# Kernel tuning notes

Measured on AMD Instinct MI355X. Metric: run time of the kernel, lower is better.

The kernel has to match this reference:

```python
import jax, jax.numpy as jnp
import numpy as np

N_NODES = 50000
N_EDGES = 800000
D = 128
BN_EPS = 1e-5
AGG_EPS = 1e-6


def setup_inputs() -> dict:
    key = jax.random.key(0)
    ks = jax.random.split(key, 20)
    s = 1.0 / np.sqrt(D)
    def w(k):
        return jax.random.normal(k, (D, D), jnp.float32) * s
    def b(k):
        return jax.random.normal(k, (D,), jnp.float32) * 0.01
    return {
        "x": jax.random.normal(ks[0], (N_NODES, D), jnp.float32),
        "e": jax.random.normal(ks[1], (N_EDGES, D), jnp.float32),
        "edge_index": jax.random.randint(ks[2], (2, N_EDGES), 0, N_NODES, jnp.int32),
        "WA": w(ks[3]), "bA": b(ks[4]),
        "WB": w(ks[5]), "bB": b(ks[6]),
        "WC": w(ks[7]), "bC": b(ks[8]),
        "WD": w(ks[9]), "bD": b(ks[10]),
        "WE": w(ks[11]), "bE": b(ks[12]),
        "gamma_x": jnp.ones((D,), jnp.float32), "beta_x": jnp.zeros((D,), jnp.float32),
        "gamma_e": jnp.ones((D,), jnp.float32), "beta_e": jnp.zeros((D,), jnp.float32),
    }


def _batchnorm(v, gamma, beta):
    # training-mode BatchNorm1d: batch stats, biased variance
    mean = v.mean(axis=0)
    var = v.var(axis=0)
    return gamma * (v - mean) * jax.lax.rsqrt(var + BN_EPS) + beta


def reference(x, e, edge_index, WA, bA, WB, bB, WC, bC, WD, bD, WE, bE,
              gamma_x, beta_x, gamma_e, beta_e):
    n_nodes = x.shape[0]
    src = edge_index[0]  # x_j (source)
    dst = edge_index[1]  # x_i (target), aggregation index

    Ax = x @ WA + bA
    Bx = x @ WB + bB
    Ce = e @ WC + bC
    Dx = x @ WD + bD
    Ex = x @ WE + bE

    # message: gather endpoints, gate
    e_ij = Dx[dst] + Ex[src] + Ce            # [n_edges, D]
    sigma_ij = jax.nn.sigmoid(e_ij)

    # aggregate: scatter-sum numerator & denominator, normalize
    num = jax.ops.segment_sum(sigma_ij * Bx[src], dst, num_segments=n_nodes)
    den = jax.ops.segment_sum(sigma_ij, dst, num_segments=n_nodes)
    aggr = num / (den + AGG_EPS)

    # update + BN + ReLU (dropout=0, residual=False per GraphGym wrapper)
    x_out = jax.nn.relu(_batchnorm(Ax + aggr, gamma_x, beta_x))
    e_out = jax.nn.relu(_batchnorm(e_ij, gamma_e, beta_e))
    return x_out, e_out
```

## Files before the change

kernel.cpp:

```cpp
#include <hip/hip_runtime.h>
#include <stdint.h>

#define DD 128
#define NB_G 2048

using f32x4  = __attribute__((ext_vector_type(4))) float;
using bf16x8 = __attribute__((ext_vector_type(8))) short;

__device__ __forceinline__ float bf2f(short u) {
  union { unsigned int i; float f; } c;
  c.i = ((unsigned int)(unsigned short)u) << 16;
  return c.f;
}
__device__ __forceinline__ short f2bf(float f) {
  union { float f; unsigned int i; } c;
  c.f = f;
  unsigned int u = c.i;
  u += 0x7fffu + ((u >> 16) & 1u);
  return (short)(u >> 16);
}

__global__ __launch_bounds__(256) void k_hist(const int* __restrict__ dst, int* __restrict__ deg, int E) {
  int e = blockIdx.x * 256 + threadIdx.x;
  if (e < E) atomicAdd(&deg[dst[e]], 1);
}

__global__ __launch_bounds__(256) void k_scan1(const int* __restrict__ deg, int* __restrict__ off,
                                               int* __restrict__ totals, int n) {
  __shared__ int sm[256];
  int t = threadIdx.x;
  int i = blockIdx.x * 256 + t;
  int v = (i < n) ? deg[i] : 0;
  sm[t] = v;
  __syncthreads();
  int acc = v;
  #pragma unroll
  for (int d = 1; d < 256; d <<= 1) {
    int add = (t >= d) ? sm[t - d] : 0;
    __syncthreads();
    acc += add;
    sm[t] = acc;
    __syncthreads();
  }
  if (i < n) off[i] = acc - v;
  if (t == 255) totals[blockIdx.x] = acc;
}

__global__ __launch_bounds__(256) void k_scan2(const int* __restrict__ totals, int* __restrict__ boff, int nb) {
  __shared__ int sm[256];
  int t = threadIdx.x;
  int v = (t < nb) ? totals[t] : 0;
  sm[t] = v;
  __syncthreads();
  int acc = v;
  #pragma unroll
  for (int d = 1; d < 256; d <<= 1) {
    int add = (t >= d) ? sm[t - d] : 0;
    __syncthreads();
    acc += add;
    sm[t] = acc;
    __syncthreads();
  }
  boff[t] = acc - v;
}

__global__ __launch_bounds__(256) void k_scan3(int* __restrict__ off, const int* __restrict__ boff,
                                               int* __restrict__ cursor, int n) {
  int i = blockIdx.x * 256 + threadIdx.x;
  if (i < n) {
    int o = off[i] + boff[blockIdx.x];
    off[i] = o;
    cursor[i] = o;
  }
}

__global__ __launch_bounds__(256) void k_fill(const int* __restrict__ dst, const int* __restrict__ src,
                                              int* __restrict__ cursor, int* __restrict__ list,
                                              int* __restrict__ srcS, int* __restrict__ posOf, int E) {
  int e = blockIdx.x * 256 + threadIdx.x;
  if (e < E) {
    int p = atomicAdd(&cursor[dst[e]], 1);
    list[p] = e;
    srcS[p] = src[e];
    posOf[e] = p;
  }
}

__global__ __launch_bounds__(256) void k_nodegemm(
    const float* __restrict__ x,
    const float* __restrict__ WA, const float* __restrict__ bA,
    const float* __restrict__ WB, const float* __restrict__ bB,
    const float* __restrict__ WD, const float* __restrict__ bD,
    const float* __restrict__ WE, const float* __restrict__ bE,
    short* __restrict__ Axh, short* __restrict__ Bxh,
    short* __restrict__ Dxh, short* __restrict__ Exh, int n) {
  __shared__ __align__(16) short xs[64][136];
  __shared__ __align__(16) short wt[128][136];
  int t = threadIdx.x;
  int m0 = blockIdx.x * 64;

  for (int i = t; i < 64 * 32; i += 256) {
    int r = i >> 5, c4 = (i & 31) * 4;
    int gr = m0 + r;
    if (gr >= n) gr = n - 1;
    float4 v = *(const float4*)&x[(size_t)gr * DD + c4];
    xs[r][c4 + 0] = f2bf(v.x); xs[r][c4 + 1] = f2bf(v.y);
    xs[r][c4 + 2] = f2bf(v.z); xs[r][c4 + 3] = f2bf(v.w);
  }

  const float* Ws[4] = {WA, WB, WD, WE};
  const float* bs[4] = {bA, bB, bD, bE};
  short* Os[4] = {Axh, Bxh, Dxh, Exh};

  int l = t & 63, w = t >> 6, lg = l >> 4, lc = l & 15;

  #pragma unroll
  for (int wi = 0; wi < 4; ++wi) {
    __syncthreads();
    {
      int c = t & 127, kb = (t >> 7) * 8;
      const float* W = Ws[wi];
      for (int p = 0; p < 8; ++p) {
        int k0 = p * 16 + kb;
        bf16x8 v;
        #pragma unroll
        for (int j = 0; j < 8; ++j) v[j] = f2bf(W[(size_t)(k0 + j) * DD + c]);
        *(bf16x8*)&wt[c][k0] = v;
      }
    }
    __syncthreads();

    f32x4 acc[8] = {};
    #pragma unroll
    for (int kk = 0; kk < 4; ++kk) {
      bf16x8 af = *(const bf16x8*)&xs[w * 16 + lc][kk * 32 + lg * 8];
      #pragma unroll
      for (int tt = 0; tt < 8; ++tt) {
        bf16x8 bfv = *(const bf16x8*)&wt[tt * 16 + lc][kk * 32 + lg * 8];
        acc[tt] = __builtin_amdgcn_mfma_f32_16x16x32_bf16(af, bfv, acc[tt], 0, 0, 0);
      }
    }
    short* O = Os[wi];
    #pragma unroll
    for (int tt = 0; tt < 8; ++tt) {
      int col = tt * 16 + lc;
      float bv = bs[wi][col];
      #pragma unroll
      for (int j = 0; j < 4; ++j) {
        int row = m0 + w * 16 + lg * 4 + j;
        if (row < n) O[(size_t)row * DD + col] = f2bf(acc[tt][j] + bv);
      }
    }
  }
}

__global__ __launch_bounds__(256) void k_edge(
    const float* __restrict__ e, const float* __restrict__ WC, const float* __restrict__ bC,
    const int* __restrict__ srcI, const int* __restrict__ dstI, const int* __restrict__ posOf,
    const short* __restrict__ Dxh, const short* __restrict__ Exh,
    short* __restrict__ eijS, int Etot) {
  __shared__ __align__(16) short es[64][136];
  __shared__ __align__(16) short wt[128][136];
  int t = threadIdx.x;
  size_t m0 = (size_t)blockIdx.x * 64;

  for (int i = t; i < 64 * 32; i += 256) {
    int r = i >> 5, c4 = (i & 31) * 4;
    size_t gr = m0 + r;
    if (gr >= (size_t)Etot) gr = Etot - 1;
    float4 v = *(const float4*)&e[gr * DD + c4];
    es[r][c4 + 0] = f2bf(v.x); es[r][c4 + 1] = f2bf(v.y);
    es[r][c4 + 2] = f2bf(v.z); es[r][c4 + 3] = f2bf(v.w);
  }
  {
    int c = t & 127, kb = (t >> 7) * 8;
    for (int p = 0; p < 8; ++p) {
      int k0 = p * 16 + kb;
      bf16x8 v;
      #pragma unroll
      for (int j = 0; j < 8; ++j) v[j] = f2bf(WC[(size_t)(k0 + j) * DD + c]);
      *(bf16x8*)&wt[c][k0] = v;
    }
  }
  __syncthreads();

  int l = t & 63, w = t >> 6, lg = l >> 4, lc = l & 15;
  f32x4 acc[8] = {};
  #pragma unroll
  for (int kk = 0; kk < 4; ++kk) {
    bf16x8 af = *(const bf16x8*)&es[w * 16 + lc][kk * 32 + lg * 8];
    #pragma unroll
    for (int tt = 0; tt < 8; ++tt) {
      bf16x8 bfv = *(const bf16x8*)&wt[tt * 16 + lc][kk * 32 + lg * 8];
      acc[tt] = __builtin_amdgcn_mfma_f32_16x16x32_bf16(af, bfv, acc[tt], 0, 0, 0);
    }
  }
  float bCv[8];
  #pragma unroll
  for (int tt = 0; tt < 8; ++tt) bCv[tt] = bC[tt * 16 + lc];

  __syncthreads();
  #pragma unroll
  for (int tt = 0; tt < 8; ++tt) {
    int col = tt * 16 + lc;
    #pragma unroll
    for (int j = 0; j < 4; ++j)
      es[w * 16 + lg * 4 + j][col] = f2bf(acc[tt][j] + bCv[tt]);
  }
  __syncthreads();

  int rr = t >> 4, cl = (t & 15) * 8;
  #pragma unroll
  for (int p = 0; p < 4; ++p) {
    int r = rr + p * 16;
    size_t edge = m0 + r;
    if (edge < (size_t)Etot) {
      int dn = dstI[edge], sn = srcI[edge], pos = posOf[edge];
      bf16x8 cv = *(const bf16x8*)&es[r][cl];
      bf16x8 dv = *(const bf16x8*)&Dxh[(size_t)dn * DD + cl];
      bf16x8 sv = *(const bf16x8*)&Exh[(size_t)sn * DD + cl];
      bf16x8 o;
      #pragma unroll
      for (int j = 0; j < 8; ++j) o[j] = f2bf(bf2f(cv[j]) + bf2f(dv[j]) + bf2f(sv[j]));
      *(bf16x8*)&eijS[(size_t)pos * DD + cl] = o;
    }
  }
}

__global__ __launch_bounds__(256) void k_gather(
    const int* __restrict__ off, const int* __restrict__ deg, const int* __restrict__ srcS,
    const short* __restrict__ eijS, const short* __restrict__ Bxh, const short* __restrict__ Axh,
    float* __restrict__ outx, float* __restrict__ pE, float* __restrict__ pX, int n) {
  int t = threadIdx.x;
  int w = t >> 6, l = t & 63;
  int qw = l >> 4, fi = l & 15;
  int waveId = blockIdx.x * 4 + w;
  const int nwaves = NB_G * 4;

  float se[8] = {}, qe[8] = {};
  float sx[4] = {}, qx[4] = {};

  for (int node = waveId; node < n; node += nwaves) {
    int start = off[node], dg = deg[node];
    float num[8] = {}, den[8] = {};
    int k = qw;
    for (; k + 4 < dg; k += 8) {
      int p0 = start + k, p1 = start + k + 4;
      int s0 = srcS[p0], s1 = srcS[p1];
      bf16x8 e0 = *(const bf16x8*)&eijS[(size_t)p0 * DD + fi * 8];
      bf16x8 e1 = *(const bf16x8*)&eijS[(size_t)p1 * DD + fi * 8];
      bf16x8 b0 = *(const bf16x8*)&Bxh[(size_t)s0 * DD + fi * 8];
      bf16x8 b1 = *(const bf16x8*)&Bxh[(size_t)s1 * DD + fi * 8];
      #pragma unroll
      for (int j = 0; j < 8; ++j) {
        float v0 = bf2f(e0[j]), v1 = bf2f(e1[j]);
        float g0 = 1.f / (1.f + __expf(-v0)), g1 = 1.f / (1.f + __expf(-v1));
        num[j] += g0 * bf2f(b0[j]) + g1 * bf2f(b1[j]);
        den[j] += g0 + g1;
        se[j] += v0 + v1; qe[j] += v0 * v0 + v1 * v1;
      }
    }
    for (; k < dg; k += 4) {
      int p0 = start + k;
      int s0 = srcS[p0];
      bf16x8 e0 = *(const bf16x8*)&eijS[(size_t)p0 * DD + fi * 8];
      bf16x8 b0 = *(const bf16x8*)&Bxh[(size_t)s0 * DD + fi * 8];
      #pragma unroll
      for (int j = 0; j < 8; ++j) {
        float v0 = bf2f(e0[j]);
        float g0 = 1.f / (1.f + __expf(-v0));
        num[j] += g0 * bf2f(b0[j]);
        den[j] += g0;
        se[j] += v0; qe[j] += v0 * v0;
      }
    }
    #pragma unroll
    for (int j = 0; j < 8; ++j) {
      num[j] += __shfl_xor(num[j], 16); num[j] += __shfl_xor(num[j], 32);
      den[j] += __shfl_xor(den[j], 16); den[j] += __shfl_xor(den[j], 32);
    }
    if (qw < 2) {
      int c0 = fi * 8 + qw * 4;
      short4 ax = *(const short4*)&Axh[(size_t)node * DD + c0];
      short axa[4] = {ax.x, ax.y, ax.z, ax.w};
      float4 o;
      float vv[4];
      #pragma unroll
      for (int j = 0; j < 4; ++j) {
        int jj = qw * 4 + j;
        float aggr = num[jj] / (den[jj] + 1e-6f);
        float xp = bf2f(axa[j]) + aggr;
        vv[j] = xp;
        sx[j] += xp; qx[j] += xp * xp;
      }
      o.x = vv[0]; o.y = vv[1]; o.z = vv[2]; o.w = vv[3];
      *(float4*)&outx[(size_t)node * DD + c0] = o;
    }
  }

  #pragma unroll
  for (int j = 0; j < 8; ++j) {
    se[j] += __shfl_xor(se[j], 16); se[j] += __shfl_xor(se[j], 32);
    qe[j] += __shfl_xor(qe[j], 16); qe[j] += __shfl_xor(qe[j], 32);
  }
  __shared__ float lsE[4][128], lqE[4][128], lsX[4][128], lqX[4][128];
  if (qw == 0) {
    #pragma unroll
    for (int j = 0; j < 8; ++j) { lsE[w][fi * 8 + j] = se[j]; lqE[w][fi * 8 + j] = qe[j]; }
  }
  if (qw < 2) {
    #pragma unroll
    for (int j = 0; j < 4; ++j) { lsX[w][fi * 8 + qw * 4 + j] = sx[j]; lqX[w][fi * 8 + qw * 4 + j] = qx[j]; }
  }
  __syncthreads();
  if (t < 128) {
    float a = lsE[0][t] + lsE[1][t] + lsE[2][t] + lsE[3][t];
    float b = lqE[0][t] + lqE[1][t] + lqE[2][t] + lqE[3][t];
    pE[(size_t)blockIdx.x * 256 + t] = a;
    pE[(size_t)blockIdx.x * 256 + 128 + t] = b;
  } else {
    int c = t - 128;
    float a = lsX[0][c] + lsX[1][c] + lsX[2][c] + lsX[3][c];
    float b = lqX[0][c] + lqX[1][c] + lqX[2][c] + lqX[3][c];
    pX[(size_t)blockIdx.x * 256 + c] = a;
    pX[(size_t)blockIdx.x * 256 + 128 + c] = b;
  }
}

__global__ __launch_bounds__(256) void k_reduce(const float* __restrict__ part, int nblk, float invcnt,
                                                const float* __restrict__ gamma, const float* __restrict__ beta,
                                                float* __restrict__ stats) {
  int c = blockIdx.x, t = threadIdx.x;
  float a = 0.f, b = 0.f;
  for (int k = t; k < nblk; k += 256) {
    a += part[(size_t)k * 256 + c];
    b += part[(size_t)k * 256 + 128 + c];
  }
  #pragma unroll
  for (int o = 32; o > 0; o >>= 1) { a += __shfl_down(a, o); b += __shfl_down(b, o); }
  __shared__ float ra[4], rb[4];
  int l = t & 63, w = t >> 6;
  if (l == 0) { ra[w] = a; rb[w] = b; }
  __syncthreads();
  if (t == 0) {
    a = ra[0] + ra[1] + ra[2] + ra[3];
    b = rb[0] + rb[1] + rb[2] + rb[3];
    float mean = a * invcnt;
    float var = b * invcnt - mean * mean;
    float istd = rsqrtf(var + 1e-5f);
    float scale = gamma[c] * istd;
    stats[c] = scale;
    stats[128 + c] = beta[c] - mean * scale;
  }
}

__global__ __launch_bounds__(256) void k_xfinal(float* __restrict__ v, const float* __restrict__ st, size_t n4) {
  size_t i = (size_t)blockIdx.x * 256 + threadIdx.x;
  if (i >= n4) return;
  float4 d = *(const float4*)&v[i * 4];
  int f0 = (int)((i * 4) & 127);
  d.x = fmaxf(0.f, d.x * st[f0 + 0] + st[128 + f0 + 0]);
  d.y = fmaxf(0.f, d.y * st[f0 + 1] + st[128 + f0 + 1]);
  d.z = fmaxf(0.f, d.z * st[f0 + 2] + st[128 + f0 + 2]);
  d.w = fmaxf(0.f, d.w * st[f0 + 3] + st[128 + f0 + 3]);
  *(float4*)&v[i * 4] = d;
}

__global__ __launch_bounds__(256) void k_efinal(const short* __restrict__ eijS, const int* __restrict__ list,
                                                const float* __restrict__ st, float* __restrict__ out, int E) {
  int t = threadIdx.x;
  int pos = blockIdx.x * 16 + (t >> 4);
  if (pos >= E) return;
  int cl = (t & 15) * 8;
  int row = list[pos];
  bf16x8 u = *(const bf16x8*)&eijS[(size_t)pos * DD + cl];
  float4 s0 = *(const float4*)&st[cl], s1 = *(const float4*)&st[cl + 4];
  float4 h0 = *(const float4*)&st[128 + cl], h1 = *(const float4*)&st[128 + cl + 4];
  float4 a, b;
  a.x = fmaxf(0.f, bf2f(u[0]) * s0.x + h0.x);
  a.y = fmaxf(0.f, bf2f(u[1]) * s0.y + h0.y);
  a.z = fmaxf(0.f, bf2f(u[2]) * s0.z + h0.z);
  a.w = fmaxf(0.f, bf2f(u[3]) * s0.w + h0.w);
  b.x = fmaxf(0.f, bf2f(u[4]) * s1.x + h1.x);
  b.y = fmaxf(0.f, bf2f(u[5]) * s1.y + h1.y);
  b.z = fmaxf(0.f, bf2f(u[6]) * s1.z + h1.z);
  b.w = fmaxf(0.f, bf2f(u[7]) * s1.w + h1.w);
  *(float4*)&out[(size_t)row * DD + cl] = a;
  *(float4*)&out[(size_t)row * DD + cl + 4] = b;
}

extern "C" void kernel_launch(void* const* d_in, const int* in_sizes, int n_in,
                              void* d_out, int out_size, void* d_ws, size_t ws_size,
                              hipStream_t stream) {
  const float* x  = (const float*)d_in[0];
  const float* e  = (const float*)d_in[1];
  const int*   ei = (const int*)d_in[2];
  const float* WA = (const float*)d_in[3];  const float* bA = (const float*)d_in[4];
  const float* WB = (const float*)d_in[5];  const float* bB = (const float*)d_in[6];
  const float* WC = (const float*)d_in[7];  const float* bC = (const float*)d_in[8];
  const float* WD = (const float*)d_in[9];  const float* bD = (const float*)d_in[10];
  const float* WE = (const float*)d_in[11]; const float* bE = (const float*)d_in[12];
  const float* gx = (const float*)d_in[13]; const float* bx = (const float*)d_in[14];
  const float* ge = (const float*)d_in[15]; const float* be = (const float*)d_in[16];

  int N = in_sizes[0] / DD;
  int E = in_sizes[2] / 2;
  const int* srcI = ei;
  const int* dstI = ei + E;

  float* outx = (float*)d_out;
  float* oute = (float*)d_out + (size_t)N * DD;

  char* wp = (char*)d_ws;
  auto alloc = [&](size_t sz) { char* p = wp; wp += (sz + 255) & ~(size_t)255; return p; };
  short* Axh    = (short*)alloc((size_t)N * DD * 2);
  short* Bxh    = (short*)alloc((size_t)N * DD * 2);
  short* Dxh    = (short*)alloc((size_t)N * DD * 2);
  short* Exh    = (short*)alloc((size_t)N * DD * 2);
  short* eijS   = (short*)alloc((size_t)E * DD * 2);
  int*   deg    = (int*)alloc((size_t)N * 4);
  int*   off    = (int*)alloc((size_t)N * 4);
  int*   cursor = (int*)alloc((size_t)N * 4);
  int*   totals = (int*)alloc(1024);
  int*   boff   = (int*)alloc(1024);
  int*   list   = (int*)alloc((size_t)E * 4);
  int*   srcS   = (int*)alloc((size_t)E * 4);
  int*   posOf  = (int*)alloc((size_t)E * 4);
  float* pE     = (float*)alloc((size_t)NB_G * 256 * 4);
  float* pX     = (float*)alloc((size_t)NB_G * 256 * 4);
  float* statsE = (float*)alloc(1024);
  float* statsX = (float*)alloc(1024);
  (void)ws_size; (void)n_in; (void)out_size;

  int nsb = (N + 255) / 256;

  hipMemsetAsync(deg, 0, (size_t)N * 4, stream);
  k_hist<<<(E + 255) / 256, 256, 0, stream>>>(dstI, deg, E);
  k_scan1<<<nsb, 256, 0, stream>>>(deg, off, totals, N);
  k_scan2<<<1, 256, 0, stream>>>(totals, boff, nsb);
  k_scan3<<<nsb, 256, 0, stream>>>(off, boff, cursor, N);
  k_fill<<<(E + 255) / 256, 256, 0, stream>>>(dstI, srcI, cursor, list, srcS, posOf, E);

  k_nodegemm<<<(N + 63) / 64, 256, 0, stream>>>(x, WA, bA, WB, bB, WD, bD, WE, bE,
                                                Axh, Bxh, Dxh, Exh, N);
  k_edge<<<(E + 63) / 64, 256, 0, stream>>>(e, WC, bC, srcI, dstI, posOf, Dxh, Exh, eijS, E);

  k_gather<<<NB_G, 256, 0, stream>>>(off, deg, srcS, eijS, Bxh, Axh, outx, pE, pX, N);
  k_reduce<<<128, 256, 0, stream>>>(pE, NB_G, 1.0f / (float)E, ge, be, statsE);
  k_reduce<<<128, 256, 0, stream>>>(pX, NB_G, 1.0f / (float)N, gx, bx, statsX);

  k_xfinal<<<(int)(((size_t)N * DD / 4 + 255) / 256), 256, 0, stream>>>(outx, statsX, (size_t)N * DD / 4);
  k_efinal<<<(E + 15) / 16, 256, 0, stream>>>(eijS, list, statsE, oute, E);
}
```

Baseline: 682.1 us.

## Pre-transpose weights to bf16 once and stream GEMM operands from global

A new small kernel converts and transposes all five weight matrices to bf16 once per call, replacing the per-block fp32-to-bf16 transpose into shared memory in the node and edge GEMMs. Both GEMM kernels now load A fragments directly from global into registers and read B fragments straight from the L2-resident transposed weights. Shared memory shrinks to a small per-wave staging buffer, so the block-wide syncthreads go away and more blocks fit per CU. The edge kernel becomes a persistent grid-stride loop over 4096 blocks. The cost is more uncoalesced global/L2 reads for the weight fragments in exchange for removing redundant conversion work and LDS pressure.

New measurement: 925.4 us. 1.36x slower.

```diff
diff --git a/kernel.cpp b/kernel.cpp
--- a/kernel.cpp
+++ b/kernel.cpp
@@ -86,144 +86,154 @@
   }
 }
 
-__global__ __launch_bounds__(256) void k_nodegemm(
+__global__ __launch_bounds__(256) void k_prewt5(
+    const float* __restrict__ WA, const float* __restrict__ WB, const float* __restrict__ WC,
+    const float* __restrict__ WD, const float* __restrict__ WE,
+    short* __restrict__ WtA, short* __restrict__ WtB, short* __restrict__ WtC,
+    short* __restrict__ WtD, short* __restrict__ WtE) {
+  const float* Ws[5] = {WA, WB, WC, WD, WE};
+  short* Os[5] = {WtA, WtB, WtC, WtD, WtE};
+  const float* W = Ws[blockIdx.x];
+  short* O = Os[blockIdx.x];
+  int t = threadIdx.x, c = t & 127, h = t >> 7;
+  for (int p = 0; p < 8; ++p) {
+    int k0 = (h * 8 + p) * 8;
+    bf16x8 v;
+    #pragma unroll
+    for (int j = 0; j < 8; ++j) v[j] = f2bf(W[(size_t)(k0 + j) * DD + c]);
+    *(bf16x8*)&O[(size_t)c * DD + k0] = v;
+  }
+}
+
+__global__ __launch_bounds__(256, 4) void k_nodegemm(
     const float* __restrict__ x,
-    const float* __restrict__ WA, const float* __restrict__ bA,
-    const float* __restrict__ WB, const float* __restrict__ bB,
-    const float* __restrict__ WD, const float* __restrict__ bD,
-    const float* __restrict__ WE, const float* __restrict__ bE,
+    const short* __restrict__ WtA, const float* __restrict__ bA,
+    const short* __restrict__ WtB, const float* __restrict__ bB,
+    const short* __restrict__ WtD, const float* __restrict__ bD,
+    const short* __restrict__ WtE, const float* __restrict__ bE,
     short* __restrict__ Axh, short* __restrict__ Bxh,
-    short* __restrict__ Dxh, short* __restrict__ Exh, int n) {
-  __shared__ __align__(16) short xs[64][136];
-  __shared__ __align__(16) short wt[128][136];
-  int t = threadIdx.x;
-  int m0 = blockIdx.x * 64;
-
-  for (int i = t; i < 64 * 32; i += 256) {
-    int r = i >> 5, c4 = (i & 31) * 4;
-    int gr = m0 + r;
-    if (gr >= n) gr = n - 1;
-    float4 v = *(const float4*)&x[(size_t)gr * DD + c4];
-    xs[r][c4 + 0] = f2bf(v.x); xs[r][c4 + 1] = f2bf(v.y);
-    xs[r][c4 + 2] = f2bf(v.z); xs[r][c4 + 3] = f2bf(v.w);
-  }
-
-  const float* Ws[4] = {WA, WB, WD, WE};
-  const float* bs[4] = {bA, bB, bD, bE};
+    short* __restrict__ Dxh, short* __restrict__ Exh, int n, int ntiles) {
+  __shared__ __align__(16) short es[4][16][136];
+  int t = threadIdx.x;
+  int w = t >> 6, l = t & 63, lg = l >> 4, lc = l & 15;
+
+  const short* Wt[4] = {WtA, WtB, WtD, WtE};
   short* Os[4] = {Axh, Bxh, Dxh, Exh};
-
-  int l = t & 63, w = t >> 6, lg = l >> 4, lc = l & 15;
-
-  #pragma unroll
-  for (int wi = 0; wi < 4; ++wi) {
-    __syncthreads();
-    {
-      int c = t & 127, kb = (t >> 7) * 8;
-      const float* W = Ws[wi];
-      for (int p = 0; p < 8; ++p) {
-        int k0 = p * 16 + kb;
-        bf16x8 v;
+  float bv[4][8];
+  #pragma unroll
+  for (int mi = 0; mi < 4; ++mi) {
+    const float* bp = (mi == 0) ? bA : (mi == 1) ? bB : (mi == 2) ? bD : bE;
+    #pragma unroll
+    for (int tt = 0; tt < 8; ++tt) bv[mi][tt] = bp[tt * 16 + lc];
+  }
+
+  for (int tile = blockIdx.x; tile < ntiles; tile += gridDim.x) {
+    int m0 = tile * 64;
+    int row = m0 + w * 16 + lc;
+    int rowc = row < n ? row : n - 1;
+    const float* xr = x + (size_t)rowc * DD;
+    bf16x8 af[4];
+    #pragma unroll
+    for (int kk = 0; kk < 4; ++kk) {
+      float4 a0 = *(const float4*)&xr[kk * 32 + lg * 8];
+      float4 a1 = *(const float4*)&xr[kk * 32 + lg * 8 + 4];
+      af[kk][0] = f2bf(a0.x); af[kk][1] = f2bf(a0.y); af[kk][2] = f2bf(a0.z); af[kk][3] = f2bf(a0.w);
+      af[kk][4] = f2bf(a1.x); af[kk][5] = f2bf(a1.y); af[kk][6] = f2bf(a1.z); af[kk][7] = f2bf(a1.w);
+    }
+    #pragma unroll
+    for (int mi = 0; mi < 4; ++mi) {
+      const short* Wm = Wt[mi];
+      f32x4 acc[8] = {};
+      #pragma unroll
+      for (int kk = 0; kk < 4; ++kk) {
         #pragma unroll
-        for (int j = 0; j < 8; ++j) v[j] = f2bf(W[(size_t)(k0 + j) * DD + c]);
-        *(bf16x8*)&wt[c][k0] = v;
-      }
-    }
-    __syncthreads();
+        for (int tt = 0; tt < 8; ++tt) {
+          bf16x8 bfv = *(const bf16x8*)&Wm[(size_t)(tt * 16 + lc) * DD + kk * 32 + lg * 8];
+          acc[tt] = __builtin_amdgcn_mfma_f32_16x16x32_bf16(af[kk], bfv, acc[tt], 0, 0, 0);
+        }
+      }
+      #pragma unroll
+      for (int tt = 0; tt < 8; ++tt) {
+        int col = tt * 16 + lc;
+        #pragma unroll
+        for (int j = 0; j < 4; ++j)
+          es[w][lg * 4 + j][col] = f2bf(acc[tt][j] + bv[mi][tt]);
+      }
+      asm volatile("s_waitcnt lgkmcnt(0)" ::: "memory");
+      __builtin_amdgcn_sched_barrier(0);
+      short* O = Os[mi];
+      #pragma unroll
+      for (int z = 0; z < 4; ++z) {
+        int r = z * 4 + lg;
+        int orow = m0 + w * 16 + r;
+        if (orow < n) {
+          bf16x8 v = *(const bf16x8*)&es[w][r][lc * 8];
+          *(bf16x8*)&O[(size_t)orow * DD + lc * 8] = v;
+        }
+      }
+      __builtin_amdgcn_sched_barrier(0);
+    }
+  }
+}
+
+__global__ __launch_bounds__(256, 4) void k_edge(
+    const float* __restrict__ e, const short* __restrict__ WtC, const float* __restrict__ bC,
+    const int* __restrict__ srcI, const int* __restrict__ dstI, const int* __restrict__ posOf,
+    const short* __restrict__ Dxh, const short* __restrict__ Exh,
+    short* __restrict__ eijS, int Etot, int ntiles) {
+  __shared__ __align__(16) short es[4][16][136];
+  int t = threadIdx.x;
+  int w = t >> 6, l = t & 63, lg = l >> 4, lc = l & 15;
+
+  float bCv[8];
+  #pragma unroll
+  for (int tt = 0; tt < 8; ++tt) bCv[tt] = bC[tt * 16 + lc];
+
+  for (int tile = blockIdx.x; tile < ntiles; tile += gridDim.x) {
+    size_t m0 = (size_t)tile * 64;
+    size_t row = m0 + w * 16 + lc;
+    size_t rowc = row < (size_t)Etot ? row : (size_t)(Etot - 1);
+    const float* er = e + rowc * DD;
 
     f32x4 acc[8] = {};
     #pragma unroll
     for (int kk = 0; kk < 4; ++kk) {
-      bf16x8 af = *(const bf16x8*)&xs[w * 16 + lc][kk * 32 + lg * 8];
+      float4 a0 = *(const float4*)&er[kk * 32 + lg * 8];
+      float4 a1 = *(const float4*)&er[kk * 32 + lg * 8 + 4];
+      bf16x8 af;
+      af[0] = f2bf(a0.x); af[1] = f2bf(a0.y); af[2] = f2bf(a0.z); af[3] = f2bf(a0.w);
+      af[4] = f2bf(a1.x); af[5] = f2bf(a1.y); af[6] = f2bf(a1.z); af[7] = f2bf(a1.w);
       #pragma unroll
       for (int tt = 0; tt < 8; ++tt) {
-        bf16x8 bfv = *(const bf16x8*)&wt[tt * 16 + lc][kk * 32 + lg * 8];
+        bf16x8 bfv = *(const bf16x8*)&WtC[(size_t)(tt * 16 + lc) * DD + kk * 32 + lg * 8];
         acc[tt] = __builtin_amdgcn_mfma_f32_16x16x32_bf16(af, bfv, acc[tt], 0, 0, 0);
       }
     }
-    short* O = Os[wi];
     #pragma unroll
     for (int tt = 0; tt < 8; ++tt) {
       int col = tt * 16 + lc;
-      float bv = bs[wi][col];
-      #pragma unroll
-      for (int j = 0; j < 4; ++j) {
-        int row = m0 + w * 16 + lg * 4 + j;
-        if (row < n) O[(size_t)row * DD + col] = f2bf(acc[tt][j] + bv);
-      }
-    }
-  }
-}
-
-__global__ __launch_bounds__(256) void k_edge(
-    const float* __restrict__ e, const float* __restrict__ WC, const float* __restrict__ bC,
-    const int* __restrict__ srcI, const int* __restrict__ dstI, const int* __restrict__ posOf,
-    const short* __restrict__ Dxh, const short* __restrict__ Exh,
-    short* __restrict__ eijS, int Etot) {
-  __shared__ __align__(16) short es[64][136];
-  __shared__ __align__(16) short wt[128][136];
-  int t = threadIdx.x;
-  size_t m0 = (size_t)blockIdx.x * 64;
-
-  for (int i = t; i < 64 * 32; i += 256) {
-    int r = i >> 5, c4 = (i & 31) * 4;
-    size_t gr = m0 + r;
-    if (gr >= (size_t)Etot) gr = Etot - 1;
-    float4 v = *(const float4*)&e[gr * DD + c4];
-    es[r][c4 + 0] = f2bf(v.x); es[r][c4 + 1] = f2bf(v.y);
-    es[r][c4 + 2] = f2bf(v.z); es[r][c4 + 3] = f2bf(v.w);
-  }
-  {
-    int c = t & 127, kb = (t >> 7) * 8;
-    for (int p = 0; p < 8; ++p) {
-      int k0 = p * 16 + kb;
-      bf16x8 v;
-      #pragma unroll
-      for (int j = 0; j < 8; ++j) v[j] = f2bf(WC[(size_t)(k0 + j) * DD + c]);
-      *(bf16x8*)&wt[c][k0] = v;
-    }
-  }
-  __syncthreads();
-
-  int l = t & 63, w = t >> 6, lg = l >> 4, lc = l & 15;
-  f32x4 acc[8] = {};
-  #pragma unroll
-  for (int kk = 0; kk < 4; ++kk) {
-    bf16x8 af = *(const bf16x8*)&es[w * 16 + lc][kk * 32 + lg * 8];
-    #pragma unroll
-    for (int tt = 0; tt < 8; ++tt) {
-      bf16x8 bfv = *(const bf16x8*)&wt[tt * 16 + lc][kk * 32 + lg * 8];
-      acc[tt] = __builtin_amdgcn_mfma_f32_16x16x32_bf16(af, bfv, acc[tt], 0, 0, 0);
-    }
-  }
-  float bCv[8];
-  #pragma unroll
-  for (int tt = 0; tt < 8; ++tt) bCv[tt] = bC[tt * 16 + lc];
-
-  __syncthreads();
-  #pragma unroll
-  for (int tt = 0; tt < 8; ++tt) {
-    int col = tt * 16 + lc;
-    #pragma unroll
-    for (int j = 0; j < 4; ++j)
-      es[w * 16 + lg * 4 + j][col] = f2bf(acc[tt][j] + bCv[tt]);
-  }
-  __syncthreads();
-
-  int rr = t >> 4, cl = (t & 15) * 8;
-  #pragma unroll
-  for (int p = 0; p < 4; ++p) {
-    int r = rr + p * 16;
-    size_t edge = m0 + r;
-    if (edge < (size_t)Etot) {
-      int dn = dstI[edge], sn = srcI[edge], pos = posOf[edge];
-      bf16x8 cv = *(const bf16x8*)&es[r][cl];
-      bf16x8 dv = *(const bf16x8*)&Dxh[(size_t)dn * DD + cl];
-      bf16x8 sv = *(const bf16x8*)&Exh[(size_t)sn * DD + cl];
-      bf16x8 o;
-      #pragma unroll
-      for (int j = 0; j < 8; ++j) o[j] = f2bf(bf2f(cv[j]) + bf2f(dv[j]) + bf2f(sv[j]));
-      *(bf16x8*)&eijS[(size_t)pos * DD + cl] = o;
-    }
+      #pragma unroll
+      for (int j = 0; j < 4; ++j)
+        es[w][lg * 4 + j][col] = f2bf(acc[tt][j] + bCv[tt]);
+    }
+    asm volatile("s_waitcnt lgkmcnt(0)" ::: "memory");
+    __builtin_amdgcn_sched_barrier(0);
+    #pragma unroll
+    for (int z = 0; z < 4; ++z) {
+      int r = z * 4 + lg;
+      size_t edge = m0 + w * 16 + r;
+      if (edge < (size_t)Etot) {
+        int pos = posOf[edge], dn = dstI[edge], sn = srcI[edge];
+        bf16x8 cv = *(const bf16x8*)&es[w][r][lc * 8];
+        bf16x8 dv = *(const bf16x8*)&Dxh[(size_t)dn * DD + lc * 8];
+        bf16x8 sv = *(const bf16x8*)&Exh[(size_t)sn * DD + lc * 8];
+        bf16x8 o;
+        #pragma unroll
+        for (int j = 0; j < 8; ++j) o[j] = f2bf(bf2f(cv[j]) + bf2f(dv[j]) + bf2f(sv[j]));
+        *(bf16x8*)&eijS[(size_t)pos * DD + lc * 8] = o;
+      }
+    }
+    __builtin_amdgcn_sched_barrier(0);
   }
 }
 
@@ -430,20 +440,28 @@
   float* pX     = (float*)alloc((size_t)NB_G * 256 * 4);
   float* statsE = (float*)alloc(1024);
   float* statsX = (float*)alloc(1024);
+  short* WtA    = (short*)alloc((size_t)DD * DD * 2);
+  short* WtB    = (short*)alloc((size_t)DD * DD * 2);
+  short* WtC    = (short*)alloc((size_t)DD * DD * 2);
+  short* WtD    = (short*)alloc((size_t)DD * DD * 2);
+  short* WtE    = (short*)alloc((size_t)DD * DD * 2);
   (void)ws_size; (void)n_in; (void)out_size;
 
   int nsb = (N + 255) / 256;
 
   hipMemsetAsync(deg, 0, (size_t)N * 4, stream);
+  k_prewt5<<<5, 256, 0, stream>>>(WA, WB, WC, WD, WE, WtA, WtB, WtC, WtD, WtE);
   k_hist<<<(E + 255) / 256, 256, 0, stream>>>(dstI, deg, E);
   k_scan1<<<nsb, 256, 0, stream>>>(deg, off, totals, N);
   k_scan2<<<1, 256, 0, stream>>>(totals, boff, nsb);
   k_scan3<<<nsb, 256, 0, stream>>>(off, boff, cursor, N);
   k_fill<<<(E + 255) / 256, 256, 0, stream>>>(dstI, srcI, cursor, list, srcS, posOf, E);
 
-  k_nodegemm<<<(N + 63) / 64, 256, 0, stream>>>(x, WA, bA, WB, bB, WD, bD, WE, bE,
-                                                Axh, Bxh, Dxh, Exh, N);
-  k_edge<<<(E + 63) / 64, 256, 0, stream>>>(e, WC, bC, srcI, dstI, posOf, Dxh, Exh, eijS, E);
+  int ntilesN = (N + 63) / 64;
+  int ntilesE = (E + 63) / 64;
+  k_nodegemm<<<ntilesN, 256, 0, stream>>>(x, WtA, bA, WtB, bB, WtD, bD, WtE, bE,
+                                          Axh, Bxh, Dxh, Exh, N, ntilesN);
+  k_edge<<<4096, 256, 0, stream>>>(e, WtC, bC, srcI, dstI, posOf, Dxh, Exh, eijS, E, ntilesE);
 
   k_gather<<<NB_G, 256, 0, stream>>>(off, deg, srcS, eijS, Bxh, Axh, outx, pE, pX, N);
   k_reduce<<<128, 256, 0, stream>>>(pE, NB_G, 1.0f / (float)E, ge, be, statsE);
```
